# Kernel optimization log

Measured on AMD Instinct MI355X. Metric: run time of the kernel, lower is better.

## Reference

```python
import jax, jax.numpy as jnp
import numpy as np

LN_EPS = 1e-5

def _layernorm(x, w, b):
    mu = jnp.mean(x, axis=-1, keepdims=True)
    var = jnp.mean(jnp.square(x - mu), axis=-1, keepdims=True)
    return (x - mu) * jax.lax.rsqrt(var + LN_EPS) * w + b

def setup_inputs() -> dict:
    key = jax.random.key(0)
    ks = jax.random.split(key, 6)
    B, NQ, QD = 8, 576, 4096
    NKV, KVD = 2304, 1024
    s = 0.02
    return {
        "x_q": jax.random.normal(ks[0], (B, NQ, QD), jnp.float32),
        "x_kv": jax.random.normal(ks[1], (B, NKV, KVD), jnp.float32),
        "q_ln_w": jnp.ones((QD,), jnp.float32),
        "q_ln_b": jnp.zeros((QD,), jnp.float32),
        "q_w": jax.random.normal(ks[2], (QD, QD), jnp.float32) * s,
        "q_b": jnp.zeros((QD,), jnp.float32),
        "k_ln_w": jnp.ones((KVD,), jnp.float32),
        "k_ln_b": jnp.zeros((KVD,), jnp.float32),
        "k_w": jax.random.normal(ks[3], (KVD, QD), jnp.float32) * s,
        "k_b": jnp.zeros((QD,), jnp.float32),
        "v_ln_w": jnp.ones((KVD,), jnp.float32),
        "v_ln_b": jnp.zeros((KVD,), jnp.float32),
        "v_w": jax.random.normal(ks[4], (KVD, QD), jnp.float32) * s,
        "v_b": jnp.zeros((QD,), jnp.float32),
    }

def reference(x_q, x_kv, q_ln_w, q_ln_b, q_w, q_b,
              k_ln_w, k_ln_b, k_w, k_b, v_ln_w, v_ln_b, v_w, v_b):
    B, NQ, QD = x_q.shape
    hw = int(round(x_kv.shape[1] ** 0.5))          # 48
    KVD = x_kv.shape[-1]
    patch_num = int(round(NQ ** 0.5))              # 24
    patch_size = hw // patch_num                   # 2
    # 'b (h w) d -> b h w d' then group into patch_num x patch_num windows
    kv = x_kv.reshape(B, hw, hw, KVD)
    kv = kv.reshape(B, patch_num, patch_size, patch_num, patch_size, KVD)
    kv = kv.transpose(0, 1, 3, 2, 4, 5).reshape(B, patch_num * patch_num, patch_size * patch_size, KVD)
    # projections (LayerNorm + Linear)
    q = _layernorm(x_q, q_ln_w, q_ln_b) @ q_w + q_b            # [B, P2, QD]
    k = _layernorm(kv, k_ln_w, k_ln_b) @ k_w + k_b             # [B, P2, S2, QD]
    v = _layernorm(kv, v_ln_w, v_ln_b) @ v_w + v_b             # [B, P2, S2, QD]
    scale = 1.0 / (QD ** 0.5)
    att = jnp.einsum('bpd,bpsd->bps', q, k) * scale            # [B, P2, S2]
    att = jnp.nan_to_num(att)
    att = jax.nn.softmax(att, axis=-1)
    feat = jnp.einsum('bps,bpsd->bpd', att, v)                 # [B, P2, QD]
    return (x_q, feat)
```

## Files before the change

### kernel.cpp

```cpp
#include <hip/hip_runtime.h>
#include <cstdint>
#include <cstddef>


typedef __attribute__((ext_vector_type(8))) short short8;
typedef __attribute__((ext_vector_type(4))) float f32x4;

#define DEV __device__ __forceinline__

DEV unsigned short f2bf(float f) {
  union { float f; unsigned u; } x; x.f = f;
  unsigned r = x.u + 0x7fffu + ((x.u >> 16) & 1u);
  return (unsigned short)(r >> 16);
}
DEV float bf2f(unsigned short u) {
  union { unsigned u; float f; } x; x.u = ((unsigned)u) << 16;
  return x.f;
}

DEV void gload16(const void* g, void* l) {
  __builtin_amdgcn_global_load_lds(
      (const __attribute__((address_space(1))) unsigned int*)g,
      (__attribute__((address_space(3))) unsigned int*)l, 16, 0, 0);
}

template <bool PARTIAL, bool OUT_BF16, bool HAS_BIAS>
__global__ __launch_bounds__(256, 2) void gemm_nt(
    const unsigned short* __restrict__ A, const unsigned short* __restrict__ Bm,
    void* __restrict__ Cv, const float* __restrict__ bias, int M, int N,
    int Kfull, int Kchunk) {
  __shared__ __align__(16) unsigned short lds_a[128 * 32];
  __shared__ __align__(16) unsigned short lds_b[128 * 32];
  const int t = threadIdx.x;
  const int l = t & 63;
  const int w = t >> 6;

  int bx = blockIdx.x, by = blockIdx.y;
  {
    const int nbx = gridDim.x, nby = gridDim.y;
    const int nwg = nbx * nby;
    int flat = by * nbx + bx;
    flat = (flat & 7) * (nwg >> 3) + (flat >> 3);
    bx = flat % nbx;
    by = flat / nbx;
  }
  const long brow = (long)bx * 128;
  const long bcol = (long)by * 128;
  const int z = blockIdx.z;
  const int k0 = z * Kchunk;

  const int srow = t >> 2;
  const int scol = (t & 3) * 8;
  const unsigned short* a0 = A + (brow + srow) * (long)Kfull + scol + k0;
  const unsigned short* a1 = A + (brow + 64 + srow) * (long)Kfull + scol + k0;
  const unsigned short* b0 = Bm + (bcol + srow) * (long)Kfull + scol + k0;
  const unsigned short* b1 = Bm + (bcol + 64 + srow) * (long)Kfull + scol + k0;
  unsigned short* la0 = lds_a + t * 8;
  unsigned short* la1 = lds_a + 2048 + t * 8;
  unsigned short* lb0 = lds_b + t * 8;
  unsigned short* lb1 = lds_b + 2048 + t * 8;

  const int wr = w >> 1, wc = w & 1;
  const int fr = l & 15;
  const int fk = (l >> 4) * 8;

  f32x4 acc[4][4] = {};

  for (int kt = 0; kt < Kchunk; kt += 32) {
    __syncthreads();
    gload16(a0 + kt, la0);
    gload16(a1 + kt, la1);
    gload16(b0 + kt, lb0);
    gload16(b1 + kt, lb1);
    asm volatile("s_waitcnt vmcnt(0)" ::: "memory");
    __syncthreads();
    short8 af[4], bfr[4];
#pragma unroll
    for (int mi = 0; mi < 4; ++mi)
      af[mi] = *(const short8*)&lds_a[(wr * 64 + mi * 16 + fr) * 32 + fk];
#pragma unroll
    for (int ni = 0; ni < 4; ++ni)
      bfr[ni] = *(const short8*)&lds_b[(wc * 64 + ni * 16 + fr) * 32 + fk];
#pragma unroll
    for (int mi = 0; mi < 4; ++mi)
#pragma unroll
      for (int ni = 0; ni < 4; ++ni)
        acc[mi][ni] = __builtin_amdgcn_mfma_f32_16x16x32_bf16(af[mi], bfr[ni],
                                                              acc[mi][ni], 0, 0, 0);
  }

  const int crow = (l >> 4) * 4;
  float* Cpart = PARTIAL ? ((float*)Cv + (size_t)z * M * (size_t)N) : nullptr;
#pragma unroll
  for (int ni = 0; ni < 4; ++ni) {
    const long col = bcol + wc * 64 + ni * 16 + fr;
    const float bv = (!PARTIAL && HAS_BIAS) ? bias[col] : 0.0f;
#pragma unroll
    for (int mi = 0; mi < 4; ++mi) {
#pragma unroll
      for (int r = 0; r < 4; ++r) {
        const long row = brow + wr * 64 + mi * 16 + crow + r;
        const float v = acc[mi][ni][r] + bv;
        if (PARTIAL)
          Cpart[row * (long)N + col] = v;
        else if (OUT_BF16)
          ((unsigned short*)Cv)[row * (long)N + col] = f2bf(v);
        else
          ((float*)Cv)[row * (long)N + col] = v;
      }
    }
  }
}

template <bool OUT_BF16, bool HAS_BIAS>
__global__ __launch_bounds__(256) void reduce_splits(
    const float* __restrict__ part, void* __restrict__ out,
    const float* __restrict__ bias, int S, size_t MN, int nmask) {
  size_t i = (size_t)blockIdx.x * 256 + threadIdx.x;
  const size_t n4 = MN / 4;
  const size_t stride = (size_t)gridDim.x * 256;
  for (; i < n4; i += stride) {
    float4 a = ((const float4*)part)[i];
    for (int s = 1; s < S; ++s) {
      const float4 b = ((const float4*)(part + (size_t)s * MN))[i];
      a.x += b.x; a.y += b.y; a.z += b.z; a.w += b.w;
    }
    if (HAS_BIAS) {
      const int c = (int)((i * 4) & (size_t)nmask);
      const float4 bv = *(const float4*)(bias + c);
      a.x += bv.x; a.y += bv.y; a.z += bv.z; a.w += bv.w;
    }
    if (OUT_BF16)
      ((ushort4*)out)[i] =
          make_ushort4(f2bf(a.x), f2bf(a.y), f2bf(a.z), f2bf(a.w));
    else
      ((float4*)out)[i] = a;
  }
}

__global__ __launch_bounds__(256) void ln_q_kernel(
    const float* __restrict__ x, const float* __restrict__ w,
    const float* __restrict__ b, float* __restrict__ copy_out,
    unsigned short* __restrict__ qn) {
  const int row = blockIdx.x, t = threadIdx.x;
  const float4* xr = (const float4*)(x + (size_t)row * 4096);
  float4 v[4];
  float s = 0.f, s2 = 0.f;
#pragma unroll
  for (int j = 0; j < 4; ++j) {
    v[j] = xr[j * 256 + t];
    s += v[j].x + v[j].y + v[j].z + v[j].w;
    s2 += v[j].x * v[j].x + v[j].y * v[j].y + v[j].z * v[j].z + v[j].w * v[j].w;
  }
#pragma unroll
  for (int off = 32; off; off >>= 1) {
    s += __shfl_xor(s, off);
    s2 += __shfl_xor(s2, off);
  }
  __shared__ float red[8];
  if ((t & 63) == 0) { red[t >> 6] = s; red[4 + (t >> 6)] = s2; }
  __syncthreads();
  s = red[0] + red[1] + red[2] + red[3];
  s2 = red[4] + red[5] + red[6] + red[7];
  const float mu = s * (1.f / 4096.f);
  const float rstd = rsqrtf(s2 * (1.f / 4096.f) - mu * mu + 1e-5f);
  float4* co = (float4*)(copy_out + (size_t)row * 4096);
  unsigned short* qr = qn + (size_t)row * 4096;
#pragma unroll
  for (int j = 0; j < 4; ++j) {
    co[j * 256 + t] = v[j];
    const int c = (j * 256 + t) * 4;
    const float4 wv = *(const float4*)(w + c);
    const float4 bv = *(const float4*)(b + c);
    ushort4 o = make_ushort4(f2bf((v[j].x - mu) * rstd * wv.x + bv.x),
                             f2bf((v[j].y - mu) * rstd * wv.y + bv.y),
                             f2bf((v[j].z - mu) * rstd * wv.z + bv.z),
                             f2bf((v[j].w - mu) * rstd * wv.w + bv.w));
    *(ushort4*)(qr + c) = o;
  }
}

__global__ __launch_bounds__(256) void ln_kv_kernel(
    const float* __restrict__ x, const float* __restrict__ kw,
    const float* __restrict__ kb, const float* __restrict__ vw,
    const float* __restrict__ vb, unsigned short* __restrict__ kn,
    unsigned short* __restrict__ vn) {
  const int row = blockIdx.x, t = threadIdx.x;
  const float4 v = ((const float4*)(x + (size_t)row * 1024))[t];
  float s = v.x + v.y + v.z + v.w;
  float s2 = v.x * v.x + v.y * v.y + v.z * v.z + v.w * v.w;
#pragma unroll
  for (int off = 32; off; off >>= 1) {
    s += __shfl_xor(s, off);
    s2 += __shfl_xor(s2, off);
  }
  __shared__ float red[8];
  if ((t & 63) == 0) { red[t >> 6] = s; red[4 + (t >> 6)] = s2; }
  __syncthreads();
  s = red[0] + red[1] + red[2] + red[3];
  s2 = red[4] + red[5] + red[6] + red[7];
  const float mu = s * (1.f / 1024.f);
  const float rstd = rsqrtf(s2 * (1.f / 1024.f) - mu * mu + 1e-5f);
  const int c = t * 4;
  const float4 kw4 = *(const float4*)(kw + c);
  const float4 kb4 = *(const float4*)(kb + c);
  const float4 vw4 = *(const float4*)(vw + c);
  const float4 vb4 = *(const float4*)(vb + c);
  const float h0 = (v.x - mu) * rstd, h1 = (v.y - mu) * rstd;
  const float h2 = (v.z - mu) * rstd, h3 = (v.w - mu) * rstd;
  *(ushort4*)(kn + (size_t)row * 1024 + c) =
      make_ushort4(f2bf(h0 * kw4.x + kb4.x), f2bf(h1 * kw4.y + kb4.y),
                   f2bf(h2 * kw4.z + kb4.z), f2bf(h3 * kw4.w + kb4.w));
  *(ushort4*)(vn + (size_t)row * 1024 + c) =
      make_ushort4(f2bf(h0 * vw4.x + vb4.x), f2bf(h1 * vw4.y + vb4.y),
                   f2bf(h2 * vw4.z + vb4.z), f2bf(h3 * vw4.w + vb4.w));
}

__global__ __launch_bounds__(256) void conv_bf16(
    const float* __restrict__ src, unsigned short* __restrict__ dst, int n4) {
  int i = blockIdx.x * 256 + threadIdx.x;
  const int stride = gridDim.x * 256;
  for (; i < n4; i += stride) {
    const float4 v = ((const float4*)src)[i];
    ((ushort4*)dst)[i] = make_ushort4(f2bf(v.x), f2bf(v.y), f2bf(v.z), f2bf(v.w));
  }
}

__global__ void transpose_conv(const float* __restrict__ src,
                               unsigned short* __restrict__ dst) {
  __shared__ float tile[32][33];
  const int n0 = blockIdx.x * 32, k0 = blockIdx.y * 32;
  const int tx = threadIdx.x, ty = threadIdx.y;
#pragma unroll
  for (int i = 0; i < 32; i += 8)
    tile[ty + i][tx] = src[(size_t)(k0 + ty + i) * 4096 + n0 + tx];
  __syncthreads();
#pragma unroll
  for (int i = 0; i < 32; i += 8)
    dst[(size_t)(n0 + ty + i) * 1024 + k0 + tx] = f2bf(tile[tx][ty + i]);
}

__global__ __launch_bounds__(256) void qkb_kernel(const float* __restrict__ qb,
                                                  const float* __restrict__ kw,
                                                  float* __restrict__ out) {
  const int c = blockIdx.x, t = threadIdx.x;
  const float4* kr = (const float4*)(kw + (size_t)c * 4096);
  const float4* q4 = (const float4*)qb;
  float s = 0.f;
#pragma unroll
  for (int j = 0; j < 4; ++j) {
    const float4 a = q4[j * 256 + t], b = kr[j * 256 + t];
    s += a.x * b.x + a.y * b.y + a.z * b.z + a.w * b.w;
  }
#pragma unroll
  for (int off = 32; off; off >>= 1) s += __shfl_xor(s, off);
  __shared__ float red[4];
  if ((t & 63) == 0) red[t >> 6] = s;
  __syncthreads();
  if (t == 0) out[c] = red[0] + red[1] + red[2] + red[3];
}

__global__ __launch_bounds__(256) void att_kernel(
    const float* __restrict__ qk, const unsigned short* __restrict__ kn,
    const unsigned short* __restrict__ vn, unsigned short* __restrict__ wkv) {
  const int m = blockIdx.x;
  const int b = m / 576, p = m % 576;
  const int py = p / 24, px = p % 24;
  const int t = threadIdx.x, w = t >> 6, l = t & 63;

  const size_t row_w =
      (size_t)b * 2304 + (size_t)(py * 2 + (w >> 1)) * 48 + (px * 2 + (w & 1));
  const float* qrow = qk + (size_t)m * 1024;
  const unsigned short* krow = kn + row_w * 1024;
  float dot = 0.f;
#pragma unroll
  for (int j = 0; j < 4; ++j) {
    const int c = j * 256 + l * 4;
    const float4 q4 = *(const float4*)(qrow + c);
    const ushort4 k4 = *(const ushort4*)(krow + c);
    dot += q4.x * bf2f(k4.x) + q4.y * bf2f(k4.y) + q4.z * bf2f(k4.z) +
           q4.w * bf2f(k4.w);
  }
#pragma unroll
  for (int off = 32; off; off >>= 1) dot += __shfl_xor(dot, off);
  __shared__ float lg[4];
  if (l == 0) lg[w] = dot * 0.015625f;
  __syncthreads();
  const float l0 = lg[0], l1 = lg[1], l2 = lg[2], l3 = lg[3];
  const float mx = fmaxf(fmaxf(l0, l1), fmaxf(l2, l3));
  float e0 = __expf(l0 - mx), e1 = __expf(l1 - mx);
  float e2 = __expf(l2 - mx), e3 = __expf(l3 - mx);
  const float inv = 1.f / (e0 + e1 + e2 + e3);
  const float at[4] = {e0 * inv, e1 * inv, e2 * inv, e3 * inv};

  const int c = t * 4;
  float a0 = 0.f, a1 = 0.f, a2 = 0.f, a3 = 0.f;
#pragma unroll
  for (int s = 0; s < 4; ++s) {
    const size_t row_s =
        (size_t)b * 2304 + (size_t)(py * 2 + (s >> 1)) * 48 + (px * 2 + (s & 1));
    const ushort4 v4 = *(const ushort4*)(vn + row_s * 1024 + c);
    a0 += at[s] * bf2f(v4.x);
    a1 += at[s] * bf2f(v4.y);
    a2 += at[s] * bf2f(v4.z);
    a3 += at[s] * bf2f(v4.w);
  }
  *(ushort4*)(wkv + (size_t)m * 1024 + c) =
      make_ushort4(f2bf(a0), f2bf(a1), f2bf(a2), f2bf(a3));
}

extern "C" void kernel_launch(void* const* d_in, const int* in_sizes, int n_in,
                              void* d_out, int out_size, void* d_ws,
                              size_t ws_size, hipStream_t stream) {
  const float* x_q = (const float*)d_in[0];
  const float* x_kv = (const float*)d_in[1];
  const float* q_ln_w = (const float*)d_in[2];
  const float* q_ln_b = (const float*)d_in[3];
  const float* q_w = (const float*)d_in[4];
  const float* q_b = (const float*)d_in[5];
  const float* k_ln_w = (const float*)d_in[6];
  const float* k_ln_b = (const float*)d_in[7];
  const float* k_w = (const float*)d_in[8];
  const float* v_ln_w = (const float*)d_in[10];
  const float* v_ln_b = (const float*)d_in[11];
  const float* v_w = (const float*)d_in[12];
  const float* v_b = (const float*)d_in[13];

  char* ws = (char*)d_ws;
  unsigned short* qn = (unsigned short*)(ws);
  unsigned short* kn = (unsigned short*)(ws + 37748736);
  unsigned short* vn = (unsigned short*)(ws + 75497472);
  unsigned short* qwb = (unsigned short*)(ws + 113246208);
  unsigned short* kwb = (unsigned short*)(ws + 146800640);
  unsigned short* Wt = (unsigned short*)(ws + 155189248);
  unsigned short* vwT = (unsigned short*)(ws + 163577856);
  float* qk = (float*)(ws + 171966464);
  float* qkbv = (float*)(ws + 190840832);
  unsigned short* wkv = (unsigned short*)(ws + 190844928);
  float* part = (float*)(ws + 200282112);

  const size_t MN_W = (size_t)1024 * 4096;
  const size_t MN_QK = (size_t)4608 * 1024;
  int splitW = 1, splitQK = 1;
  if (ws_size >= 200282112 + 4 * MN_QK * 4) { splitW = 4; splitQK = 4; }
  else if (ws_size >= 200282112 + 2 * MN_QK * 4) { splitW = 2; splitQK = 2; }
  const bool partial_ok = ws_size >= 200282112 + MN_QK * 4;

  float* out0 = (float*)d_out;
  float* out1 = out0 + (size_t)4608 * 4096;

  ln_q_kernel<<<4608, 256, 0, stream>>>(x_q, q_ln_w, q_ln_b, out0, qn);
  ln_kv_kernel<<<18432, 256, 0, stream>>>(x_kv, k_ln_w, k_ln_b, v_ln_w, v_ln_b,
                                          kn, vn);
  conv_bf16<<<4096, 256, 0, stream>>>(q_w, qwb, 4096 * 4096 / 4);
  conv_bf16<<<1024, 256, 0, stream>>>(k_w, kwb, 1024 * 4096 / 4);
  transpose_conv<<<dim3(128, 32), dim3(32, 8), 0, stream>>>(v_w, vwT);
  qkb_kernel<<<1024, 256, 0, stream>>>(q_b, k_w, qkbv);

  if (partial_ok) {
    gemm_nt<true, false, false><<<dim3(8, 32, splitW), 256, 0, stream>>>(
        kwb, qwb, part, nullptr, 1024, 4096, 4096, 4096 / splitW);
    reduce_splits<true, false><<<2048, 256, 0, stream>>>(part, Wt, nullptr,
                                                         splitW, MN_W, 0);
    gemm_nt<true, false, false><<<dim3(36, 8, splitQK), 256, 0, stream>>>(
        qn, Wt, part, nullptr, 4608, 1024, 4096, 4096 / splitQK);
    reduce_splits<false, true><<<2048, 256, 0, stream>>>(part, qk, qkbv,
                                                         splitQK, MN_QK, 1023);
  } else {
    gemm_nt<false, true, false><<<dim3(8, 32), 256, 0, stream>>>(
        kwb, qwb, Wt, nullptr, 1024, 4096, 4096, 4096);
    gemm_nt<false, false, true><<<dim3(36, 8), 256, 0, stream>>>(
        qn, Wt, qk, qkbv, 4608, 1024, 4096, 4096);
  }

  att_kernel<<<4608, 256, 0, stream>>>(qk, kn, vn, wkv);
  gemm_nt<false, false, true><<<dim3(36, 32), 256, 0, stream>>>(
      wkv, vwT, out1, v_b, 4608, 4096, 1024, 1024);
}
```

Measured before the change: 603.8 us.

## Double GEMM K-tile with XOR-swizzled LDS and fuse split-K reduce into attention

The GEMM kernel now stages 64-wide K tiles instead of 32, using an XOR swizzle on the LDS layout to avoid bank conflicts, which halves the barrier and wait count per K. The split-K reduction and bias add for the q·Wk product are folded into the attention kernel, removing one launch and a full fp32 write/read of the qk matrix. The split factor for the weight-product GEMM drops to 2, and the unsplit fallback path is removed, so the code now always assumes the partial workspace exists.

```diff
diff --git a/kernel.cpp b/kernel.cpp
--- a/kernel.cpp
+++ b/kernel.cpp
@@ -29,8 +29,8 @@
     const unsigned short* __restrict__ A, const unsigned short* __restrict__ Bm,
     void* __restrict__ Cv, const float* __restrict__ bias, int M, int N,
     int Kfull, int Kchunk) {
-  __shared__ __align__(16) unsigned short lds_a[128 * 32];
-  __shared__ __align__(16) unsigned short lds_b[128 * 32];
+  __shared__ __align__(16) unsigned short lds_a[128 * 64];
+  __shared__ __align__(16) unsigned short lds_b[128 * 64];
   const int t = threadIdx.x;
   const int l = t & 63;
   const int w = t >> 6;
@@ -49,44 +49,54 @@
   const int z = blockIdx.z;
   const int k0 = z * Kchunk;
 
-  const int srow = t >> 2;
-  const int scol = (t & 3) * 8;
-  const unsigned short* a0 = A + (brow + srow) * (long)Kfull + scol + k0;
-  const unsigned short* a1 = A + (brow + 64 + srow) * (long)Kfull + scol + k0;
-  const unsigned short* b0 = Bm + (bcol + srow) * (long)Kfull + scol + k0;
-  const unsigned short* b1 = Bm + (bcol + 64 + srow) * (long)Kfull + scol + k0;
-  unsigned short* la0 = lds_a + t * 8;
-  unsigned short* la1 = lds_a + 2048 + t * 8;
-  unsigned short* lb0 = lds_b + t * 8;
-  unsigned short* lb1 = lds_b + 2048 + t * 8;
+  const int srow0 = t >> 3;
+  const int gsrc = (t & 7) ^ ((t >> 3) & 7);
+  const unsigned short* aS[4];
+  const unsigned short* bS[4];
+  unsigned short* aD[4];
+  unsigned short* bD[4];
+#pragma unroll
+  for (int j = 0; j < 4; ++j) {
+    const long row = srow0 + 32 * j;
+    aS[j] = A + (brow + row) * (long)Kfull + k0 + gsrc * 8;
+    bS[j] = Bm + (bcol + row) * (long)Kfull + k0 + gsrc * 8;
+    aD[j] = lds_a + (t + 256 * j) * 8;
+    bD[j] = lds_b + (t + 256 * j) * 8;
+  }
 
   const int wr = w >> 1, wc = w & 1;
   const int fr = l & 15;
-  const int fk = (l >> 4) * 8;
+  const int xr = fr & 7;
+  const int gq0 = l >> 4;
 
   f32x4 acc[4][4] = {};
 
-  for (int kt = 0; kt < Kchunk; kt += 32) {
+  for (int kt = 0; kt < Kchunk; kt += 64) {
     __syncthreads();
-    gload16(a0 + kt, la0);
-    gload16(a1 + kt, la1);
-    gload16(b0 + kt, lb0);
-    gload16(b1 + kt, lb1);
+#pragma unroll
+    for (int j = 0; j < 4; ++j) {
+      gload16(aS[j] + kt, aD[j]);
+      gload16(bS[j] + kt, bD[j]);
+    }
     asm volatile("s_waitcnt vmcnt(0)" ::: "memory");
     __syncthreads();
-    short8 af[4], bfr[4];
-#pragma unroll
-    for (int mi = 0; mi < 4; ++mi)
-      af[mi] = *(const short8*)&lds_a[(wr * 64 + mi * 16 + fr) * 32 + fk];
-#pragma unroll
-    for (int ni = 0; ni < 4; ++ni)
-      bfr[ni] = *(const short8*)&lds_b[(wc * 64 + ni * 16 + fr) * 32 + fk];
-#pragma unroll
-    for (int mi = 0; mi < 4; ++mi)
+#pragma unroll
+    for (int ks = 0; ks < 2; ++ks) {
+      const int gx = ((ks * 4 + gq0) ^ xr) * 8;
+      short8 af[4], bfr[4];
+#pragma unroll
+      for (int mi = 0; mi < 4; ++mi)
+        af[mi] = *(const short8*)&lds_a[(wr * 64 + mi * 16 + fr) * 64 + gx];
 #pragma unroll
       for (int ni = 0; ni < 4; ++ni)
-        acc[mi][ni] = __builtin_amdgcn_mfma_f32_16x16x32_bf16(af[mi], bfr[ni],
-                                                              acc[mi][ni], 0, 0, 0);
+        bfr[ni] = *(const short8*)&lds_b[(wc * 64 + ni * 16 + fr) * 64 + gx];
+#pragma unroll
+      for (int mi = 0; mi < 4; ++mi)
+#pragma unroll
+        for (int ni = 0; ni < 4; ++ni)
+          acc[mi][ni] = __builtin_amdgcn_mfma_f32_16x16x32_bf16(
+              af[mi], bfr[ni], acc[mi][ni], 0, 0, 0);
+    }
   }
 
   const int crow = (l >> 4) * 4;
@@ -112,10 +122,9 @@
   }
 }
 
-template <bool OUT_BF16, bool HAS_BIAS>
-__global__ __launch_bounds__(256) void reduce_splits(
-    const float* __restrict__ part, void* __restrict__ out,
-    const float* __restrict__ bias, int S, size_t MN, int nmask) {
+__global__ __launch_bounds__(256) void reduce_splits_bf16(
+    const float* __restrict__ part, unsigned short* __restrict__ out, int S,
+    size_t MN) {
   size_t i = (size_t)blockIdx.x * 256 + threadIdx.x;
   const size_t n4 = MN / 4;
   const size_t stride = (size_t)gridDim.x * 256;
@@ -125,16 +134,8 @@
       const float4 b = ((const float4*)(part + (size_t)s * MN))[i];
       a.x += b.x; a.y += b.y; a.z += b.z; a.w += b.w;
     }
-    if (HAS_BIAS) {
-      const int c = (int)((i * 4) & (size_t)nmask);
-      const float4 bv = *(const float4*)(bias + c);
-      a.x += bv.x; a.y += bv.y; a.z += bv.z; a.w += bv.w;
-    }
-    if (OUT_BF16)
-      ((ushort4*)out)[i] =
-          make_ushort4(f2bf(a.x), f2bf(a.y), f2bf(a.z), f2bf(a.w));
-    else
-      ((float4*)out)[i] = a;
+    ((ushort4*)out)[i] =
+        make_ushort4(f2bf(a.x), f2bf(a.y), f2bf(a.z), f2bf(a.w));
   }
 }
 
@@ -260,52 +261,70 @@
   if (t == 0) out[c] = red[0] + red[1] + red[2] + red[3];
 }
 
-__global__ __launch_bounds__(256) void att_kernel(
-    const float* __restrict__ qk, const unsigned short* __restrict__ kn,
+__global__ __launch_bounds__(256) void att_fused(
+    const float* __restrict__ part, int S, size_t PMN,
+    const float* __restrict__ qkb, const unsigned short* __restrict__ kn,
     const unsigned short* __restrict__ vn, unsigned short* __restrict__ wkv) {
   const int m = blockIdx.x;
   const int b = m / 576, p = m % 576;
   const int py = p / 24, px = p % 24;
   const int t = threadIdx.x, w = t >> 6, l = t & 63;
-
-  const size_t row_w =
-      (size_t)b * 2304 + (size_t)(py * 2 + (w >> 1)) * 48 + (px * 2 + (w & 1));
-  const float* qrow = qk + (size_t)m * 1024;
-  const unsigned short* krow = kn + row_w * 1024;
-  float dot = 0.f;
-#pragma unroll
-  for (int j = 0; j < 4; ++j) {
-    const int c = j * 256 + l * 4;
-    const float4 q4 = *(const float4*)(qrow + c);
-    const ushort4 k4 = *(const ushort4*)(krow + c);
-    dot += q4.x * bf2f(k4.x) + q4.y * bf2f(k4.y) + q4.z * bf2f(k4.z) +
-           q4.w * bf2f(k4.w);
-  }
-#pragma unroll
-  for (int off = 32; off; off >>= 1) dot += __shfl_xor(dot, off);
-  __shared__ float lg[4];
-  if (l == 0) lg[w] = dot * 0.015625f;
-  __syncthreads();
-  const float l0 = lg[0], l1 = lg[1], l2 = lg[2], l3 = lg[3];
-  const float mx = fmaxf(fmaxf(l0, l1), fmaxf(l2, l3));
-  float e0 = __expf(l0 - mx), e1 = __expf(l1 - mx);
-  float e2 = __expf(l2 - mx), e3 = __expf(l3 - mx);
-  const float inv = 1.f / (e0 + e1 + e2 + e3);
-  const float at[4] = {e0 * inv, e1 * inv, e2 * inv, e3 * inv};
-
   const int c = t * 4;
+  const size_t off = (size_t)m * 1024 + c;
+
+  float4 q = *(const float4*)(part + off);
+  for (int s = 1; s < S; ++s) {
+    const float4 pp = *(const float4*)(part + (size_t)s * PMN + off);
+    q.x += pp.x; q.y += pp.y; q.z += pp.z; q.w += pp.w;
+  }
+  const float4 qb4 = *(const float4*)(qkb + c);
+  q.x += qb4.x; q.y += qb4.y; q.z += qb4.z; q.w += qb4.w;
+
+  size_t rows[4];
+#pragma unroll
+  for (int s = 0; s < 4; ++s)
+    rows[s] = ((size_t)b * 2304 + (size_t)(py * 2 + (s >> 1)) * 48 +
+               (px * 2 + (s & 1))) * 1024;
+
+  float dot[4];
+#pragma unroll
+  for (int s = 0; s < 4; ++s) {
+    const ushort4 k4 = *(const ushort4*)(kn + rows[s] + c);
+    dot[s] = q.x * bf2f(k4.x) + q.y * bf2f(k4.y) + q.z * bf2f(k4.z) +
+             q.w * bf2f(k4.w);
+  }
+#pragma unroll
+  for (int s = 0; s < 4; ++s)
+#pragma unroll
+    for (int o = 32; o; o >>= 1) dot[s] += __shfl_xor(dot[s], o);
+
+  __shared__ float red[4][4];
+  if (l == 0) {
+#pragma unroll
+    for (int s = 0; s < 4; ++s) red[w][s] = dot[s];
+  }
+  __syncthreads();
+  float lg[4];
+#pragma unroll
+  for (int s = 0; s < 4; ++s)
+    lg[s] = (red[0][s] + red[1][s] + red[2][s] + red[3][s]) * 0.015625f;
+  const float mx = fmaxf(fmaxf(lg[0], lg[1]), fmaxf(lg[2], lg[3]));
+  float e[4];
+#pragma unroll
+  for (int s = 0; s < 4; ++s) e[s] = __expf(lg[s] - mx);
+  const float inv = 1.f / (e[0] + e[1] + e[2] + e[3]);
+
   float a0 = 0.f, a1 = 0.f, a2 = 0.f, a3 = 0.f;
 #pragma unroll
   for (int s = 0; s < 4; ++s) {
-    const size_t row_s =
-        (size_t)b * 2304 + (size_t)(py * 2 + (s >> 1)) * 48 + (px * 2 + (s & 1));
-    const ushort4 v4 = *(const ushort4*)(vn + row_s * 1024 + c);
-    a0 += at[s] * bf2f(v4.x);
-    a1 += at[s] * bf2f(v4.y);
-    a2 += at[s] * bf2f(v4.z);
-    a3 += at[s] * bf2f(v4.w);
-  }
-  *(ushort4*)(wkv + (size_t)m * 1024 + c) =
+    const float at = e[s] * inv;
+    const ushort4 v4 = *(const ushort4*)(vn + rows[s] + c);
+    a0 += at * bf2f(v4.x);
+    a1 += at * bf2f(v4.y);
+    a2 += at * bf2f(v4.z);
+    a3 += at * bf2f(v4.w);
+  }
+  *(ushort4*)(wkv + off) =
       make_ushort4(f2bf(a0), f2bf(a1), f2bf(a2), f2bf(a3));
 }
 
@@ -334,7 +353,6 @@
   unsigned short* kwb = (unsigned short*)(ws + 146800640);
   unsigned short* Wt = (unsigned short*)(ws + 155189248);
   unsigned short* vwT = (unsigned short*)(ws + 163577856);
-  float* qk = (float*)(ws + 171966464);
   float* qkbv = (float*)(ws + 190840832);
   unsigned short* wkv = (unsigned short*)(ws + 190844928);
   float* part = (float*)(ws + 200282112);
@@ -342,9 +360,8 @@
   const size_t MN_W = (size_t)1024 * 4096;
   const size_t MN_QK = (size_t)4608 * 1024;
   int splitW = 1, splitQK = 1;
-  if (ws_size >= 200282112 + 4 * MN_QK * 4) { splitW = 4; splitQK = 4; }
-  else if (ws_size >= 200282112 + 2 * MN_QK * 4) { splitW = 2; splitQK = 2; }
-  const bool partial_ok = ws_size >= 200282112 + MN_QK * 4;
+  if (ws_size >= 200282112ull + 4 * MN_QK * 4) { splitW = 2; splitQK = 4; }
+  else if (ws_size >= 200282112ull + 2 * MN_QK * 4) { splitW = 2; splitQK = 2; }
 
   float* out0 = (float*)d_out;
   float* out1 = out0 + (size_t)4608 * 4096;
@@ -357,23 +374,14 @@
   transpose_conv<<<dim3(128, 32), dim3(32, 8), 0, stream>>>(v_w, vwT);
   qkb_kernel<<<1024, 256, 0, stream>>>(q_b, k_w, qkbv);
 
-  if (partial_ok) {
-    gemm_nt<true, false, false><<<dim3(8, 32, splitW), 256, 0, stream>>>(
-        kwb, qwb, part, nullptr, 1024, 4096, 4096, 4096 / splitW);
-    reduce_splits<true, false><<<2048, 256, 0, stream>>>(part, Wt, nullptr,
-                                                         splitW, MN_W, 0);
-    gemm_nt<true, false, false><<<dim3(36, 8, splitQK), 256, 0, stream>>>(
-        qn, Wt, part, nullptr, 4608, 1024, 4096, 4096 / splitQK);
-    reduce_splits<false, true><<<2048, 256, 0, stream>>>(part, qk, qkbv,
-                                                         splitQK, MN_QK, 1023);
-  } else {
-    gemm_nt<false, true, false><<<dim3(8, 32), 256, 0, stream>>>(
-        kwb, qwb, Wt, nullptr, 1024, 4096, 4096, 4096);
-    gemm_nt<false, false, true><<<dim3(36, 8), 256, 0, stream>>>(
-        qn, Wt, qk, qkbv, 4608, 1024, 4096, 4096);
-  }
-
-  att_kernel<<<4608, 256, 0, stream>>>(qk, kn, vn, wkv);
+  gemm_nt<true, false, false><<<dim3(8, 32, splitW), 256, 0, stream>>>(
+      kwb, qwb, part, nullptr, 1024, 4096, 4096, 4096 / splitW);
+  reduce_splits_bf16<<<2048, 256, 0, stream>>>(part, Wt, splitW, MN_W);
+
+  gemm_nt<true, false, false><<<dim3(36, 8, splitQK), 256, 0, stream>>>(
+      qn, Wt, part, nullptr, 4608, 1024, 4096, 4096 / splitQK);
+  att_fused<<<4608, 256, 0, stream>>>(part, splitQK, MN_QK, qkbv, kn, vn, wkv);
+
   gemm_nt<false, false, true><<<dim3(36, 32), 256, 0, stream>>>(
       wkv, vwT, out1, v_b, 4608, 4096, 1024, 1024);
 }
```

Measured after the change: 560.5 us. -7.2%, faster.
